# Performance work log

Measured on AMD Instinct MI355X. Metric: run time of the kernel, lower is better.

## Reference

```python
import jax, jax.numpy as jnp
import numpy as np

H = 16        # attention heads
KVH = 4       # kv heads (GQA)
D = 128       # qk head_dim = qk_nope(64) + qk_rope(64)
ROPE = 64     # rotary sub-dim
VCH = 128     # v_channels
HID = 2048    # hidden size
E = 8         # routed experts
K = 2         # top-k
EPS = 1e-6
THETA = 10000.0


def rmsnorm(x, w):
    return x * jax.lax.rsqrt(jnp.mean(x * x, axis=-1, keepdims=True) + EPS) * w


def apply_rope(x, pos):
    # x: [T, h, ROPE]; rotate-half convention on the rope sub-dim
    half = ROPE // 2
    inv_freq = 1.0 / (THETA ** (jnp.arange(half, dtype=jnp.float32) / half))
    ang = pos.astype(jnp.float32)[:, None] * inv_freq          # [T, half]
    cos = jnp.cos(ang)[:, None, :]
    sin = jnp.sin(ang)[:, None, :]
    x1, x2 = x[..., :half], x[..., half:]
    return jnp.concatenate([x1 * cos - x2 * sin, x1 * sin + x2 * cos], axis=-1)


def swiglu(x, w_gate, w_up, w_down):
    return (jax.nn.silu(x @ w_gate) * (x @ w_up)) @ w_down


def setup_inputs() -> dict:
    key = jax.random.key(0)
    ks = jax.random.split(key, 16)
    T = 2048
    sc = 0.02
    n = lambda k, s: jax.random.normal(k, s, dtype=jnp.float32) * sc
    return {
        "x": jax.random.normal(ks[0], (T, HID), dtype=jnp.float32),
        "positions": jnp.arange(T, dtype=jnp.int32),
        "ln1_w": jnp.ones((HID,), jnp.float32),
        "qkv_w": n(ks[1], (HID, H * D + KVH * D + KVH * VCH)),
        "qkv_b": n(ks[2], (H * D + KVH * D + KVH * VCH,)),
        "k_ln_w": jnp.ones((D,), jnp.float32),
        "o_w": n(ks[3], (H * VCH, HID)),
        "ln2_w": jnp.ones((HID,), jnp.float32),
        "router_w": n(ks[4], (HID, E)),
        "w1": n(ks[5], (E, HID, 512)),
        "w2": n(ks[6], (E, 512, HID)),
        "w3": n(ks[7], (E, HID, 512)),
        "sw1": n(ks[8], (HID, 1024)),
        "sw2": n(ks[9], (1024, HID)),
        "sw3": n(ks[10], (HID, 1024)),
    }


def reference(x, positions, ln1_w, qkv_w, qkv_b, k_ln_w, o_w, ln2_w,
              router_w, w1, w2, w3, sw1, sw2, sw3):
    T = x.shape[0]
    # --- attention block ---
    h = rmsnorm(x, ln1_w)
    qkv = h @ qkv_w + qkv_b
    q = qkv[:, : H * D].reshape(T, H, D)
    k = qkv[:, H * D : H * D + KVH * D].reshape(T, KVH, D)
    v = qkv[:, H * D + KVH * D :].reshape(T, KVH, VCH)
    k = rmsnorm(k, k_ln_w)  # per-head k_layernorm over head_dim
    # rope applied to the trailing qk_rope_dim of q/k
    q = jnp.concatenate([q[..., : D - ROPE], apply_rope(q[..., D - ROPE :], positions)], -1)
    k = jnp.concatenate([k[..., : D - ROPE], apply_rope(k[..., D - ROPE :], positions)], -1)
    rep = H // KVH
    kf = jnp.repeat(k, rep, axis=1)   # [T, H, D]
    vf = jnp.repeat(v, rep, axis=1)   # [T, H, VCH]
    scale = D ** -0.5
    scores = jnp.einsum("qhd,khd->hqk", q, kf) * scale
    causal = jnp.tril(jnp.ones((T, T), dtype=bool))
    scores = jnp.where(causal[None], scores, jnp.float32(-1e30))
    p = jax.nn.softmax(scores, axis=-1)
    attn = jnp.einsum("hqk,khv->qhv", p, vf).reshape(T, H * VCH)
    x = x + attn @ o_w
    # --- MoE block: shared expert + top-k routed experts ---
    h2 = rmsnorm(x, ln2_w)
    probs = jax.nn.softmax(h2 @ router_w, axis=-1)            # [T, E]
    topw, topi = jax.lax.top_k(probs, K)
    topw = topw / jnp.sum(topw, axis=-1, keepdims=True)        # renormalize top-k
    combine = jnp.sum(jax.nn.one_hot(topi, E, dtype=h2.dtype) * topw[..., None], axis=1)  # [T, E]
    moe = swiglu(h2, sw1, sw3, sw2)                            # shared expert
    for e in range(E):  # small fixed expert count
        moe = moe + combine[:, e : e + 1] * swiglu(h2, w1[e], w3[e], w2[e])
    return x + moe
```

## Files before the change

### kernel.cpp

```cpp
#include <hip/hip_runtime.h>


typedef _Float16 half_t;
typedef _Float16 half8 __attribute__((ext_vector_type(8)));
typedef float    f32x4 __attribute__((ext_vector_type(4)));
typedef float    floatx4 __attribute__((ext_vector_type(4)));

#define T_TOK 2048
#define HIDN  2048
#define NH    16
#define NKVH  4
#define HD    128
#define QKV_N 3072
#define NEXP  8

#define MFMA16(a,b,c) __builtin_amdgcn_mfma_f32_16x16x32_f16(a,b,c,0,0,0)

__device__ __forceinline__ void gload_lds16(const half_t* g, half_t* l) {
    __builtin_amdgcn_global_load_lds(
        (const __attribute__((address_space(1))) void*)g,
        (__attribute__((address_space(3))) void*)l, 16, 0, 0);
}

__global__ __launch_bounds__(256)
void rmsnorm_split_k(const float* __restrict__ x, const float* __restrict__ w,
                     half_t* __restrict__ hi, half_t* __restrict__ lo)
{
    const int row = blockIdx.x, tid = threadIdx.x;
    const float* xr = x + (size_t)row * HIDN;
    floatx4 v0 = *(const floatx4*)(xr + tid * 8);
    floatx4 v1 = *(const floatx4*)(xr + tid * 8 + 4);
    float ss = v0[0]*v0[0] + v0[1]*v0[1] + v0[2]*v0[2] + v0[3]*v0[3]
             + v1[0]*v1[0] + v1[1]*v1[1] + v1[2]*v1[2] + v1[3]*v1[3];
    for (int o = 32; o; o >>= 1) ss += __shfl_down(ss, o);
    __shared__ float red[4];
    if ((tid & 63) == 0) red[tid >> 6] = ss;
    __syncthreads();
    ss = red[0] + red[1] + red[2] + red[3];
    float rs = rsqrtf(ss * (1.0f / HIDN) + 1e-6f);
    floatx4 w0 = *(const floatx4*)(w + tid * 8);
    floatx4 w1 = *(const floatx4*)(w + tid * 8 + 4);
    float vv[8] = { v0[0]*w0[0], v0[1]*w0[1], v0[2]*w0[2], v0[3]*w0[3],
                    v1[0]*w1[0], v1[1]*w1[1], v1[2]*w1[2], v1[3]*w1[3] };
    half8 hv, lv;
#pragma unroll
    for (int j = 0; j < 8; ++j) {
        float o = vv[j] * rs;
        half_t h = (half_t)o;
        hv[j] = h;
        lv[j] = (half_t)((o - (float)h) * 1024.0f);
    }
    *(half8*)(hi + (size_t)row * HIDN + tid * 8) = hv;
    if (lo) *(half8*)(lo + (size_t)row * HIDN + tid * 8) = lv;
}

__global__ __launch_bounds__(256)
void transpose_split2(const float* __restrict__ src, half_t* __restrict__ dh,
                      half_t* __restrict__ dl, int sstride, int dstride)
{
    __shared__ float tile[32][36];
    const int n0 = blockIdx.x * 32, k0 = blockIdx.y * 32;
    const int tid = threadIdx.x;
    {
        int r = tid >> 3, c = (tid & 7) * 4;
        *(floatx4*)&tile[r][c] =
            *(const floatx4*)(src + (size_t)(k0 + r) * sstride + n0 + c);
    }
    __syncthreads();
    int n = tid & 31, g = tid >> 5, gg = g & 3;
    half8 hv;
    if (g < 4) {
#pragma unroll
        for (int j = 0; j < 8; ++j) hv[j] = (half_t)tile[gg * 8 + j][n];
        *(half8*)(dh + (size_t)(n0 + n) * dstride + k0 + gg * 8) = hv;
    } else {
#pragma unroll
        for (int j = 0; j < 8; ++j) {
            float v = tile[gg * 8 + j][n];
            half_t h = (half_t)v;
            hv[j] = (half_t)((v - (float)h) * 1024.0f);
        }
        *(half8*)(dl + (size_t)(n0 + n) * dstride + k0 + gg * 8) = hv;
    }
}

__global__ __launch_bounds__(256)
void transpose_f16(const float* __restrict__ src, half_t* __restrict__ dh,
                   int sstride, int dstride)
{
    __shared__ float tile[32][68];
    const int n0 = blockIdx.x * 64, k0 = blockIdx.y * 32;
    const int tid = threadIdx.x;
    {
        int r = tid >> 3, c = (tid & 7) * 4;
        const float* s = src + (size_t)(k0 + r) * sstride + n0;
        *(floatx4*)&tile[r][c]      = *(const floatx4*)(s + c);
        *(floatx4*)&tile[r][c + 32] = *(const floatx4*)(s + c + 32);
    }
    __syncthreads();
    int n = tid & 63, g = tid >> 6;
    half8 hv;
#pragma unroll
    for (int j = 0; j < 8; ++j) hv[j] = (half_t)tile[g * 8 + j][n];
    *(half8*)(dh + (size_t)(n0 + n) * dstride + k0 + g * 8) = hv;
}

__global__ __launch_bounds__(256)
void w13_transpose(const float* __restrict__ sw1, const float* __restrict__ w1,
                   const float* __restrict__ sw3, const float* __restrict__ w3,
                   half_t* __restrict__ dst)
{
    __shared__ float tile[32][68];
    const int n0 = blockIdx.x * 64, k0 = blockIdx.y * 32;
    const int tid = threadIdx.x;
    const float* base;
    int stride;
    if (n0 < 1024)      { base = sw1 + n0; stride = 1024; }
    else if (n0 < 5120) { int e = (n0 - 1024) >> 9;
                          base = w1 + (size_t)e * HIDN * 512 + ((n0 - 1024) & 511);
                          stride = 512; }
    else if (n0 < 6144) { base = sw3 + (n0 - 5120); stride = 1024; }
    else                { int e = (n0 - 6144) >> 9;
                          base = w3 + (size_t)e * HIDN * 512 + ((n0 - 6144) & 511);
                          stride = 512; }
    {
        int r = tid >> 3, c = (tid & 7) * 4;
        const float* s = base + (size_t)(k0 + r) * stride;
        *(floatx4*)&tile[r][c]      = *(const floatx4*)(s + c);
        *(floatx4*)&tile[r][c + 32] = *(const floatx4*)(s + c + 32);
    }
    __syncthreads();
    int n = tid & 63, g = tid >> 6;
    half8 hv;
#pragma unroll
    for (int j = 0; j < 8; ++j) hv[j] = (half_t)tile[g * 8 + j][n];
    *(half8*)(dst + (size_t)(n0 + n) * HIDN + k0 + g * 8) = hv;
}

__global__ __launch_bounds__(256)
void w2_transpose(const float* __restrict__ sw2, const float* __restrict__ w2,
                  half_t* __restrict__ dst)
{
    __shared__ float tile[32][68];
    const int n0 = blockIdx.x * 64, k0 = blockIdx.y * 32;
    const int tid = threadIdx.x;
    {
        int r = tid >> 3, c = (tid & 7) * 4;
        int k = k0 + r;
        const float* s;
        if (k < 1024) s = sw2 + (size_t)k * HIDN + n0;
        else {
            int e = (k - 1024) >> 9, kk = (k - 1024) & 511;
            s = w2 + ((size_t)e * 512 + kk) * HIDN + n0;
        }
        *(floatx4*)&tile[r][c]      = *(const floatx4*)(s + c);
        *(floatx4*)&tile[r][c + 32] = *(const floatx4*)(s + c + 32);
    }
    __syncthreads();
    int n = tid & 63, g = tid >> 6;
    half8 hv;
#pragma unroll
    for (int j = 0; j < 8; ++j) hv[j] = (half_t)tile[g * 8 + j][n];
    *(half8*)(dst + (size_t)(n0 + n) * 5120 + k0 + g * 8) = hv;
}

__global__ __launch_bounds__(256)
void owu_kernel(const float* __restrict__ ow, const float* __restrict__ ln2w,
                const float* __restrict__ rw, float* __restrict__ owu)
{
    const int k = blockIdx.x * 4 + (threadIdx.x >> 6);
    const int lane = threadIdx.x & 63;
    float acc[NEXP] = {};
    const float* row = ow + (size_t)k * HIDN;
#pragma unroll
    for (int j = 0; j < 8; ++j) {
        int c = j * 256 + lane * 4;
        floatx4 ov = *(const floatx4*)(row + c);
        floatx4 lw = *(const floatx4*)(ln2w + c);
#pragma unroll
        for (int i = 0; i < 4; ++i) {
            float s = ov[i] * lw[i];
            const float* rwc = rw + (size_t)(c + i) * NEXP;
#pragma unroll
            for (int e = 0; e < NEXP; ++e) acc[e] += s * rwc[e];
        }
    }
#pragma unroll
    for (int e = 0; e < NEXP; ++e)
        for (int o = 32; o; o >>= 1) acc[e] += __shfl_down(acc[e], o);
    if (lane == 0) {
#pragma unroll
        for (int e = 0; e < NEXP; ++e) owu[(size_t)k * NEXP + e] = acc[e];
    }
}

template<bool SPLIT, int BM>
__global__ __launch_bounds__(256, 2)
void gemm_f16(const half_t* __restrict__ Ah, const half_t* __restrict__ Al,
              const half_t* __restrict__ Bth, const half_t* __restrict__ Btl,
              const float* __restrict__ bias, const float* __restrict__ res,
              float* __restrict__ Cf, half_t* __restrict__ Ch,
              int M, int N, int K)
{
    constexpr int NBUF = SPLIT ? 2 : 1;
    constexpr int MR = BM / 32;
    __shared__ half_t As[NBUF][BM * 32];
    __shared__ half_t Bs[NBUF][128 * 32];
    const int tid = threadIdx.x, lane = tid & 63, wid = tid >> 6;
    const int l15 = lane & 15, l4 = lane >> 4;
    const int row0 = blockIdx.y * BM, col0 = blockIdx.x * 128;
    const int wr = (wid >> 1) * (BM / 2), wc = (wid & 1) * 64;
    f32x4 accM[MR][4] = {}, accC[MR][4] = {};
    const int lrw = lane >> 2, lcl = (lane & 3) * 8;

    for (int k0 = 0; k0 < K; k0 += 32) {
        __syncthreads();
#pragma unroll
        for (int j = 0; j < BM / 64; ++j) {
            const int r = wid * (BM / 4) + j * 16;
            const size_t ga = (size_t)(row0 + r + lrw) * K + k0 + lcl;
            gload_lds16(Ah + ga, &As[0][r * 32]);
            if constexpr (SPLIT) gload_lds16(Al + ga, &As[1][r * 32]);
        }
#pragma unroll
        for (int j = 0; j < 2; ++j) {
            const int r = wid * 32 + j * 16;
            const size_t gb = (size_t)(col0 + r + lrw) * K + k0 + lcl;
            gload_lds16(Bth + gb, &Bs[0][r * 32]);
            if constexpr (SPLIT) gload_lds16(Btl + gb, &Bs[1][r * 32]);
        }
        __syncthreads();
        half8 ah[MR], al[MR], bh[4], bl[4];
#pragma unroll
        for (int m = 0; m < MR; ++m) {
            int off = (wr + m * 16 + l15) * 32 + l4 * 8;
            ah[m] = *(const half8*)&As[0][off];
            if constexpr (SPLIT) al[m] = *(const half8*)&As[1][off];
        }
#pragma unroll
        for (int n = 0; n < 4; ++n) {
            int off = (wc + n * 16 + l15) * 32 + l4 * 8;
            bh[n] = *(const half8*)&Bs[0][off];
            if constexpr (SPLIT) bl[n] = *(const half8*)&Bs[1][off];
        }
#pragma unroll
        for (int m = 0; m < MR; ++m)
#pragma unroll
            for (int n = 0; n < 4; ++n) {
                accM[m][n] = MFMA16(ah[m], bh[n], accM[m][n]);
                if constexpr (SPLIT) {
                    accC[m][n] = MFMA16(ah[m], bl[n], accC[m][n]);
                    accC[m][n] = MFMA16(al[m], bh[n], accC[m][n]);
                }
            }
    }
#pragma unroll
    for (int m = 0; m < MR; ++m) {
#pragma unroll
        for (int n = 0; n < 4; ++n) {
            int gr0 = row0 + wr + m * 16 + l4 * 4;
            int gc  = col0 + wc + n * 16 + l15;
            float b = bias ? bias[gc] : 0.0f;
#pragma unroll
            for (int i = 0; i < 4; ++i) {
                float v = accM[m][n][i];
                if constexpr (SPLIT) v += accC[m][n][i] * (1.0f / 1024.0f);
                v += b;
                size_t idx = (size_t)(gr0 + i) * N + gc;
                if (res) v += res[idx];
                if (Cf) Cf[idx] = v;
                if (Ch) Ch[idx] = (half_t)v;
            }
        }
    }
}

__global__ __launch_bounds__(256)
void qkv_prep(const float* __restrict__ qkv, const int* __restrict__ pos,
              const float* __restrict__ klnw,
              half_t* __restrict__ qh, half_t* __restrict__ ql,
              half_t* __restrict__ kh, half_t* __restrict__ kl)
{
    const int t = blockIdx.x, tid = threadIdx.x, lane = tid & 63, wid = tid >> 6;
    const float* row = qkv + (size_t)t * QKV_N;
    __shared__ float cs[32], sn[32];
    if (tid < 32) {
        double freq = exp((double)tid * -0.28782313662425572);
        double ang = (double)pos[t] * freq;
        const double twopi = 6.283185307179586476925286766559;
        ang -= twopi * floor(ang * (1.0 / twopi));
        float a = (float)ang;
        cs[tid] = cosf(a);
        sn[tid] = sinf(a);
    }
    __syncthreads();

    const float qscale = 0.08838834764831845f;
    {
        const int hh = tid >> 4, d0 = (tid & 15) * 8;
        const float* qrow = row + hh * HD;
        float outv[8];
        if (d0 < 64) {
#pragma unroll
            for (int j = 0; j < 8; ++j) outv[j] = qrow[d0 + j];
        } else if (d0 < 96) {
            int j0 = d0 - 64;
#pragma unroll
            for (int j = 0; j < 8; ++j) {
                int jj = j0 + j;
                outv[j] = qrow[64 + jj] * cs[jj] - qrow[96 + jj] * sn[jj];
            }
        } else {
            int j0 = d0 - 96;
#pragma unroll
            for (int j = 0; j < 8; ++j) {
                int jj = j0 + j;
                outv[j] = qrow[64 + jj] * sn[jj] + qrow[96 + jj] * cs[jj];
            }
        }
        half8 hv, lv;
#pragma unroll
        for (int j = 0; j < 8; ++j) {
            float o = outv[j] * qscale;
            half_t h = (half_t)o;
            hv[j] = h;
            lv[j] = (half_t)((o - (float)h) * 1024.0f);
        }
        size_t base = (size_t)t * (NH * HD) + hh * HD + d0;
        *(half8*)(qh + base) = hv;
        *(half8*)(ql + base) = lv;
    }
    {
        const float* krow = row + NH * HD + wid * HD;
        float a0 = krow[lane], a1 = krow[64 + lane];
        float ss = a0 * a0 + a1 * a1;
        for (int o = 32; o; o >>= 1) ss += __shfl_down(ss, o);
        ss = __shfl(ss, 0);
        float rs = rsqrtf(ss * (1.0f / HD) + 1e-6f);
        float n0 = a0 * rs * klnw[lane];
        float n1 = a1 * rs * klnw[64 + lane];
        float other = __shfl_xor(n1, 32);
        int j = lane & 31;
        float o1 = (lane < 32) ? (n1 * cs[j] - other * sn[j])
                               : (other * sn[j] + n1 * cs[j]);
        size_t base = (size_t)t * (NKVH * HD) + wid * HD;
        half_t h;
        h = (half_t)n0; kh[base + lane] = h;
        kl[base + lane] = (half_t)((n0 - (float)h) * 1024.0f);
        h = (half_t)o1; kh[base + 64 + lane] = h;
        kl[base + 64 + lane] = (half_t)((o1 - (float)h) * 1024.0f);
    }
}

__global__ __launch_bounds__(256, 2)
void attn_kernel(const half_t* __restrict__ qh, const half_t* __restrict__ ql,
                 const half_t* __restrict__ kh, const half_t* __restrict__ kl,
                 const half_t* __restrict__ vth, const half_t* __restrict__ vtl,
                 half_t* __restrict__ oh, half_t* __restrict__ ol)
{
    const int bid = blockIdx.x;
    const int qblk = 31 - (bid >> 4);
    const int h = bid & 15;
    const int kvh = h >> 2;
    const int tid = threadIdx.x, lane = tid & 63, wid = tid >> 6;
    const int q0 = qblk * 64 + wid * 16;
    const int l15 = lane & 15, l4 = lane >> 4;

    __shared__ half_t Ksh[32][136], Ksl[32][136];
    __shared__ half_t Vsh[128][40], Vsl[128][40];
    __shared__ half_t Ph[4][16][40], Pl[4][16][40];

    half8 qfh[4], qfl[4];
    {
        const size_t qb = (size_t)(q0 + l15) * (NH * HD) + h * HD + l4 * 8;
#pragma unroll
        for (int c = 0; c < 4; ++c) {
            qfh[c] = *(const half8*)(qh + qb + c * 32);
            qfl[c] = *(const half8*)(ql + qb + c * 32);
        }
    }

    f32x4 om[8] = {}, oc[8] = {};
    float mrow[4] = { -1e30f, -1e30f, -1e30f, -1e30f };
    float lrow[4] = {};

    const int kr = tid >> 4, kc = (tid & 15) * 8;
    const int vd = tid >> 2, vc = (tid & 3) * 8;
    uint4 rk0h, rk1h, rk0l, rk1l, rv0h, rv1h, rv0l, rv1l;

    const int kvend = qblk * 64 + 64;

#define LOAD_TILE(KV0)                                                        \
    do {                                                                      \
        size_t sk0 = (size_t)((KV0) + kr) * (NKVH * HD) + kvh * HD + kc;      \
        size_t sk1 = sk0 + (size_t)16 * (NKVH * HD);                          \
        rk0h = *(const uint4*)(kh + sk0);  rk0l = *(const uint4*)(kl + sk0);  \
        rk1h = *(const uint4*)(kh + sk1);  rk1l = *(const uint4*)(kl + sk1);  \
        size_t sv0 = (size_t)(kvh * HD + vd) * T_TOK + (KV0) + vc;            \
        size_t sv1 = sv0 + (size_t)64 * T_TOK;                                \
        rv0h = *(const uint4*)(vth + sv0); rv0l = *(const uint4*)(vtl + sv0); \
        rv1h = *(const uint4*)(vth + sv1); rv1l = *(const uint4*)(vtl + sv1); \
    } while (0)

    LOAD_TILE(0);
    for (int kv0 = 0; kv0 < kvend; kv0 += 32) {
        *(uint4*)&Ksh[kr][kc]      = rk0h;  *(uint4*)&Ksl[kr][kc]      = rk0l;
        *(uint4*)&Ksh[kr + 16][kc] = rk1h;  *(uint4*)&Ksl[kr + 16][kc] = rk1l;
        *(uint4*)&Vsh[vd][vc]      = rv0h;  *(uint4*)&Vsl[vd][vc]      = rv0l;
        *(uint4*)&Vsh[vd + 64][vc] = rv1h;  *(uint4*)&Vsl[vd + 64][vc] = rv1l;
        __syncthreads();
        if (kv0 + 32 < kvend) LOAD_TILE(kv0 + 32);

        f32x4 sf[2];
        __builtin_amdgcn_s_setprio(1);
#pragma unroll
        for (int t2 = 0; t2 < 2; ++t2) {
            f32x4 s = {}, sc = {};
#pragma unroll
            for (int c = 0; c < 4; ++c) {
                half8 bh = *(const half8*)&Ksh[t2 * 16 + l15][c * 32 + l4 * 8];
                half8 bl = *(const half8*)&Ksl[t2 * 16 + l15][c * 32 + l4 * 8];
                s  = MFMA16(qfh[c], bh, s);
                sc = MFMA16(qfh[c], bl, sc);
                sc = MFMA16(qfl[c], bh, sc);
            }
            sf[t2] = s + sc * (1.0f / 1024.0f);
        }
        __builtin_amdgcn_s_setprio(0);

        float pmax[4];
#pragma unroll
        for (int i = 0; i < 4; ++i) {
            const int qg = q0 + l4 * 4 + i;
#pragma unroll
            for (int t2 = 0; t2 < 2; ++t2) {
                int kvg = kv0 + t2 * 16 + l15;
                if (kvg > qg) sf[t2][i] = -1e30f;
            }
            float mx = fmaxf(sf[0][i], sf[1][i]);
#pragma unroll
            for (int o = 1; o < 16; o <<= 1) mx = fmaxf(mx, __shfl_xor(mx, o));
            pmax[i] = mx;
        }
        float dm = fmaxf(fmaxf(pmax[0] - mrow[0], pmax[1] - mrow[1]),
                         fmaxf(pmax[2] - mrow[2], pmax[3] - mrow[3]));
        if (__any(dm > 6.0f)) {
#pragma unroll
            for (int i = 0; i < 4; ++i) {
                float mnew = fmaxf(mrow[i], pmax[i]);
                float resc = expf(mrow[i] - mnew);
                lrow[i] *= resc;
#pragma unroll
                for (int c8 = 0; c8 < 8; ++c8) {
                    om[c8][i] *= resc; oc[c8][i] *= resc;
                }
                mrow[i] = mnew;
            }
        }
#pragma unroll
        for (int i = 0; i < 4; ++i) {
            float p0 = expf(sf[0][i] - mrow[i]);
            float p1 = expf(sf[1][i] - mrow[i]);
            lrow[i] += p0 + p1;
            half_t hh;
            hh = (half_t)p0;
            Ph[wid][l4 * 4 + i][l15] = hh;
            Pl[wid][l4 * 4 + i][l15] = (half_t)((p0 - (float)hh) * 1024.0f);
            hh = (half_t)p1;
            Ph[wid][l4 * 4 + i][16 + l15] = hh;
            Pl[wid][l4 * 4 + i][16 + l15] = (half_t)((p1 - (float)hh) * 1024.0f);
        }

        half8 pah = *(const half8*)&Ph[wid][l15][l4 * 8];
        half8 pal = *(const half8*)&Pl[wid][l15][l4 * 8];
        __builtin_amdgcn_s_setprio(1);
#pragma unroll
        for (int c8 = 0; c8 < 8; ++c8) {
            half8 vh = *(const half8*)&Vsh[c8 * 16 + l15][l4 * 8];
            half8 vl = *(const half8*)&Vsl[c8 * 16 + l15][l4 * 8];
            om[c8] = MFMA16(pah, vh, om[c8]);
            oc[c8] = MFMA16(pah, vl, oc[c8]);
            oc[c8] = MFMA16(pal, vh, oc[c8]);
        }
        __builtin_amdgcn_s_setprio(0);
        __syncthreads();
    }
#undef LOAD_TILE

#pragma unroll
    for (int i = 0; i < 4; ++i)
#pragma unroll
        for (int o = 1; o < 16; o <<= 1) lrow[i] += __shfl_xor(lrow[i], o);

#pragma unroll
    for (int c8 = 0; c8 < 8; ++c8) {
#pragma unroll
        for (int i = 0; i < 4; ++i) {
            float v = (om[c8][i] + oc[c8][i] * (1.0f / 1024.0f)) / lrow[i];
            size_t idx = (size_t)(q0 + l4 * 4 + i) * (NH * HD) + h * HD + c8 * 16 + l15;
            half_t hh = (half_t)v;
            oh[idx] = hh;
            ol[idx] = (half_t)((v - (float)hh) * 1024.0f);
        }
    }
}

__global__ __launch_bounds__(256)
void router_linear(const float* __restrict__ x, const half_t* __restrict__ ah,
                   const half_t* __restrict__ al, const float* __restrict__ x2,
                   const float* __restrict__ ln2w, const float* __restrict__ rw,
                   const float* __restrict__ owu, float* __restrict__ combine)
{
    const int t = blockIdx.x, tid = threadIdx.x;
    const float* xr2 = x2 + (size_t)t * HIDN;
    float ss = 0.0f;
#pragma unroll
    for (int i = 0; i < 8; ++i) {
        float v = xr2[tid + i * 256];
        ss += v * v;
    }
    for (int o = 32; o; o >>= 1) ss += __shfl_down(ss, o);
    __shared__ float red[4];
    if ((tid & 63) == 0) red[tid >> 6] = ss;
    __syncthreads();
    ss = red[0] + red[1] + red[2] + red[3];
    float rs = rsqrtf(ss * (1.0f / HIDN) + 1e-6f);

    const float* xr = x + (size_t)t * HIDN;
    const half_t* ar = ah + (size_t)t * HIDN;
    const half_t* alr = al + (size_t)t * HIDN;
    float acc[NEXP] = {};
#pragma unroll
    for (int i = 0; i < 8; ++i) {
        int c = tid + i * 256;
        float xv = xr[c] * ln2w[c];
        float ap = (float)ar[c] + (float)alr[c] * (1.0f / 1024.0f);
        const float* rwc = rw + (size_t)c * NEXP;
        const float* owc = owu + (size_t)c * NEXP;
#pragma unroll
        for (int e = 0; e < NEXP; ++e) acc[e] += xv * rwc[e] + ap * owc[e];
    }
#pragma unroll
    for (int e = 0; e < NEXP; ++e)
        for (int o = 32; o; o >>= 1) acc[e] += __shfl_down(acc[e], o);
    __shared__ float red8[4][NEXP];
    if ((tid & 63) == 0)
#pragma unroll
        for (int e = 0; e < NEXP; ++e) red8[tid >> 6][e] = acc[e];
    __syncthreads();
    if (tid == 0) {
        float lg[NEXP];
#pragma unroll
        for (int e = 0; e < NEXP; ++e)
            lg[e] = (red8[0][e] + red8[1][e] + red8[2][e] + red8[3][e]) * rs;
        int i1 = 0;
        for (int e = 1; e < NEXP; ++e) if (lg[e] > lg[i1]) i1 = e;
        int i2 = (i1 == 0) ? 1 : 0;
        for (int e = 0; e < NEXP; ++e) if (e != i1 && lg[e] > lg[i2]) i2 = e;
        float mx = lg[i1];
        float p1 = expf(lg[i1] - mx), p2 = expf(lg[i2] - mx);
        float inv = 1.0f / (p1 + p2);
        float* cr = combine + (size_t)t * NEXP;
#pragma unroll
        for (int e = 0; e < NEXP; ++e) cr[e] = 0.0f;
        cr[i1] = p1 * inv;
        cr[i2] = p2 * inv;
    }
}

__global__ __launch_bounds__(256)
void moe_act(const half_t* __restrict__ GU, const float* __restrict__ comb,
             half_t* __restrict__ Abig)
{
    int idx = blockIdx.x * 256 + threadIdx.x;
    int t = idx / 640, c8 = idx % 640;
    int n = c8 * 8;
    half8 g8 = *(const half8*)(GU + (size_t)t * 10240 + n);
    half8 u8 = *(const half8*)(GU + (size_t)t * 10240 + 5120 + n);
    float sc = (n < 1024) ? 1.0f : comb[(size_t)t * NEXP + ((n - 1024) >> 9)];
    half8 o8;
#pragma unroll
    for (int j = 0; j < 8; ++j) {
        float g = (float)g8[j], u = (float)u8[j];
        float s = g / (1.0f + expf(-g));
        o8[j] = (half_t)(s * u * sc);
    }
    *(half8*)(Abig + (size_t)t * 5120 + n) = o8;
}

extern "C" void kernel_launch(void* const* d_in, const int* in_sizes, int n_in,
                              void* d_out, int out_size, void* d_ws, size_t ws_size,
                              hipStream_t stream)
{
    (void)in_sizes; (void)n_in; (void)out_size; (void)ws_size;
    const float* x    = (const float*)d_in[0];
    const int*   pos  = (const int*)  d_in[1];
    const float* ln1w = (const float*)d_in[2];
    const float* qkvw = (const float*)d_in[3];
    const float* qkvb = (const float*)d_in[4];
    const float* klnw = (const float*)d_in[5];
    const float* ow   = (const float*)d_in[6];
    const float* ln2w = (const float*)d_in[7];
    const float* rw   = (const float*)d_in[8];
    const float* w1   = (const float*)d_in[9];
    const float* w2   = (const float*)d_in[10];
    const float* w3   = (const float*)d_in[11];
    const float* sw1  = (const float*)d_in[12];
    const float* sw2  = (const float*)d_in[13];
    const float* sw3  = (const float*)d_in[14];
    float* out = (float*)d_out;

    char* ws = (char*)d_ws;
    const size_t AB = 16842752;
    float*  x2      = (float*)(ws);
    float*  combine = (float*)(ws + 16777216);
    half_t* h_hi    = (half_t*)(ws + AB);
    half_t* h_lo    = (half_t*)(ws + AB + 8388608);
    half_t* qkvwt_h = (half_t*)(ws + AB + 16777216);
    half_t* qkvwt_l = (half_t*)(ws + AB + 29360128);
    float*  qkv     = (float*)(ws + AB + 41943040);
    half_t* q_h     = (half_t*)(ws + AB + 67108864);
    half_t* q_l     = (half_t*)(ws + AB + 75497472);
    half_t* k_h     = (half_t*)(ws + AB + 83886080);
    half_t* k_l     = (half_t*)(ws + AB + 85983232);
    half_t* vt_h    = (half_t*)(ws + AB + 88080384);
    half_t* vt_l    = (half_t*)(ws + AB + 90177536);
    half_t* attn_h  = (half_t*)(ws + AB);
    half_t* attn_l  = (half_t*)(ws + AB + 8388608);
    half_t* owt     = (half_t*)(ws + AB + 16777216);
    float*  ow_u    = (float*)(ws + AB + 25165824);
    half_t* h2      = (half_t*)(ws + AB + 33554432);
    half_t* W13t    = (half_t*)(ws + AB + 41943040);
    half_t* GU      = (half_t*)(ws + AB + 83886080);
    half_t* Abig    = (half_t*)(ws + AB);
    half_t* W2t     = (half_t*)(ws + AB + 41943040);

    dim3 b256(256);

    rmsnorm_split_k<<<T_TOK, b256, 0, stream>>>(x, ln1w, h_hi, h_lo);
    transpose_split2<<<dim3(QKV_N / 32, HIDN / 32), b256, 0, stream>>>(
        qkvw, qkvwt_h, qkvwt_l, QKV_N, HIDN);
    gemm_f16<true, 64><<<dim3(QKV_N / 128, T_TOK / 64), b256, 0, stream>>>(
        h_hi, h_lo, qkvwt_h, qkvwt_l, qkvb, nullptr, qkv, nullptr,
        T_TOK, QKV_N, HIDN);
    qkv_prep<<<T_TOK, b256, 0, stream>>>(qkv, pos, klnw, q_h, q_l, k_h, k_l);
    transpose_split2<<<dim3(512 / 32, T_TOK / 32), b256, 0, stream>>>(
        qkv + 2560, vt_h, vt_l, QKV_N, T_TOK);
    transpose_f16<<<dim3(HIDN / 64, HIDN / 32), b256, 0, stream>>>(
        ow, owt, HIDN, HIDN);
    owu_kernel<<<512, b256, 0, stream>>>(ow, ln2w, rw, ow_u);
    attn_kernel<<<512, b256, 0, stream>>>(
        q_h, q_l, k_h, k_l, vt_h, vt_l, attn_h, attn_l);
    gemm_f16<false, 64><<<dim3(HIDN / 128, T_TOK / 64), b256, 0, stream>>>(
        attn_h, nullptr, owt, nullptr, nullptr, x, x2, nullptr,
        T_TOK, HIDN, HIDN);
    router_linear<<<T_TOK, b256, 0, stream>>>(
        x, attn_h, attn_l, x2, ln2w, rw, ow_u, combine);
    rmsnorm_split_k<<<T_TOK, b256, 0, stream>>>(x2, ln2w, h2, nullptr);
    w13_transpose<<<dim3(10240 / 64, HIDN / 32), b256, 0, stream>>>(
        sw1, w1, sw3, w3, W13t);
    gemm_f16<false, 128><<<dim3(10240 / 128, T_TOK / 128), b256, 0, stream>>>(
        h2, nullptr, W13t, nullptr, nullptr, nullptr, nullptr, GU,
        T_TOK, 10240, HIDN);
    w2_transpose<<<dim3(HIDN / 64, 5120 / 32), b256, 0, stream>>>(sw2, w2, W2t);
    moe_act<<<(T_TOK * 640) / 256, b256, 0, stream>>>(GU, combine, Abig);
    gemm_f16<false, 64><<<dim3(HIDN / 128, T_TOK / 64), b256, 0, stream>>>(
        Abig, nullptr, W2t, nullptr, nullptr, x2, out, nullptr,
        T_TOK, HIDN, 5120);
}
```

Baseline: 648.9 us.

## Double-buffer GEMM LDS loads and split causal attention over KV chunks

The GEMM kernel now double-buffers its LDS tiles so the next K-slice's global-to-LDS load is issued before the current slice's MFMAs, and it takes an occupancy template parameter. Attention is split-K over 512-wide KV chunks. Later query blocks are spread across up to 4 blocks, which balances causal work across 1280 blocks, and a new combine kernel merges the partials with log-sum-exp rescaling. The split adds fp32 partial traffic, an extra launch, and workspace aliasing that could conflict with other buffers. Launch bounds also change for attention and some GEMMs, which affects register pressure.

```diff
diff --git a/kernel.cpp b/kernel.cpp
--- a/kernel.cpp
+++ b/kernel.cpp
@@ -194,8 +194,8 @@
     }
 }
 
-template<bool SPLIT, int BM>
-__global__ __launch_bounds__(256, 2)
+template<bool SPLIT, int BM, int WPE>
+__global__ __launch_bounds__(256, WPE)
 void gemm_f16(const half_t* __restrict__ Ah, const half_t* __restrict__ Al,
               const half_t* __restrict__ Bth, const half_t* __restrict__ Btl,
               const float* __restrict__ bias, const float* __restrict__ res,
@@ -204,8 +204,8 @@
 {
     constexpr int NBUF = SPLIT ? 2 : 1;
     constexpr int MR = BM / 32;
-    __shared__ half_t As[NBUF][BM * 32];
-    __shared__ half_t Bs[NBUF][128 * 32];
+    __shared__ half_t As[2][NBUF][BM * 32];
+    __shared__ half_t Bs[2][NBUF][128 * 32];
     const int tid = threadIdx.x, lane = tid & 63, wid = tid >> 6;
     const int l15 = lane & 15, l4 = lane >> 4;
     const int row0 = blockIdx.y * BM, col0 = blockIdx.x * 128;
@@ -213,35 +213,41 @@
     f32x4 accM[MR][4] = {}, accC[MR][4] = {};
     const int lrw = lane >> 2, lcl = (lane & 3) * 8;
 
-    for (int k0 = 0; k0 < K; k0 += 32) {
-        __syncthreads();
-#pragma unroll
-        for (int j = 0; j < BM / 64; ++j) {
-            const int r = wid * (BM / 4) + j * 16;
-            const size_t ga = (size_t)(row0 + r + lrw) * K + k0 + lcl;
-            gload_lds16(Ah + ga, &As[0][r * 32]);
-            if constexpr (SPLIT) gload_lds16(Al + ga, &As[1][r * 32]);
-        }
-#pragma unroll
-        for (int j = 0; j < 2; ++j) {
-            const int r = wid * 32 + j * 16;
-            const size_t gb = (size_t)(col0 + r + lrw) * K + k0 + lcl;
-            gload_lds16(Bth + gb, &Bs[0][r * 32]);
-            if constexpr (SPLIT) gload_lds16(Btl + gb, &Bs[1][r * 32]);
-        }
-        __syncthreads();
+#define STAGE(BUF, K0)                                                        \
+    do {                                                                      \
+        _Pragma("unroll")                                                     \
+        for (int j = 0; j < BM / 64; ++j) {                                   \
+            const int r = wid * (BM / 4) + j * 16;                            \
+            const size_t ga = (size_t)(row0 + r + lrw) * K + (K0) + lcl;      \
+            gload_lds16(Ah + ga, &As[BUF][0][r * 32]);                        \
+            if constexpr (SPLIT) gload_lds16(Al + ga, &As[BUF][1][r * 32]);   \
+        }                                                                     \
+        _Pragma("unroll")                                                     \
+        for (int j = 0; j < 2; ++j) {                                         \
+            const int r = wid * 32 + j * 16;                                  \
+            const size_t gb = (size_t)(col0 + r + lrw) * K + (K0) + lcl;      \
+            gload_lds16(Bth + gb, &Bs[BUF][0][r * 32]);                       \
+            if constexpr (SPLIT) gload_lds16(Btl + gb, &Bs[BUF][1][r * 32]);  \
+        }                                                                     \
+    } while (0)
+
+    STAGE(0, 0);
+    __syncthreads();
+    int cur = 0;
+    for (int k0 = 0; k0 < K; k0 += 32, cur ^= 1) {
+        if (k0 + 32 < K) STAGE(cur ^ 1, k0 + 32);
         half8 ah[MR], al[MR], bh[4], bl[4];
 #pragma unroll
         for (int m = 0; m < MR; ++m) {
             int off = (wr + m * 16 + l15) * 32 + l4 * 8;
-            ah[m] = *(const half8*)&As[0][off];
-            if constexpr (SPLIT) al[m] = *(const half8*)&As[1][off];
+            ah[m] = *(const half8*)&As[cur][0][off];
+            if constexpr (SPLIT) al[m] = *(const half8*)&As[cur][1][off];
         }
 #pragma unroll
         for (int n = 0; n < 4; ++n) {
             int off = (wc + n * 16 + l15) * 32 + l4 * 8;
-            bh[n] = *(const half8*)&Bs[0][off];
-            if constexpr (SPLIT) bl[n] = *(const half8*)&Bs[1][off];
+            bh[n] = *(const half8*)&Bs[cur][0][off];
+            if constexpr (SPLIT) bl[n] = *(const half8*)&Bs[cur][1][off];
         }
 #pragma unroll
         for (int m = 0; m < MR; ++m)
@@ -253,7 +259,10 @@
                     accC[m][n] = MFMA16(al[m], bh[n], accC[m][n]);
                 }
             }
-    }
+        __syncthreads();
+    }
+#undef STAGE
+
 #pragma unroll
     for (int m = 0; m < MR; ++m) {
 #pragma unroll
@@ -352,18 +361,28 @@
     }
 }
 
-__global__ __launch_bounds__(256, 2)
+__global__ __launch_bounds__(256, 3)
 void attn_kernel(const half_t* __restrict__ qh, const half_t* __restrict__ ql,
                  const half_t* __restrict__ kh, const half_t* __restrict__ kl,
                  const half_t* __restrict__ vth, const half_t* __restrict__ vtl,
-                 half_t* __restrict__ oh, half_t* __restrict__ ol)
+                 half_t* __restrict__ oh, half_t* __restrict__ ol,
+                 float* __restrict__ Op0, float* __restrict__ Op1,
+                 float* __restrict__ ml)
 {
     const int bid = blockIdx.x;
-    const int qblk = 31 - (bid >> 4);
-    const int h = bid & 15;
+    const int h = bid & 15, r = bid >> 4;
+    int q, c;
+    if (r < 8)       { q = r;                 c = 0; }
+    else if (r < 24) { q = 8 + ((r - 8) >> 1);  c = (r - 8) & 1; }
+    else if (r < 48) { q = 16 + (r - 24) / 3;   c = (r - 24) % 3; }
+    else             { q = 24 + ((r - 48) >> 2); c = (r - 48) & 3; }
+    const int nch = (q < 8) ? 1 : (q < 16) ? 2 : (q < 24) ? 3 : 4;
+    const int kvbeg = c * 512;
+    const int kvend = min(kvbeg + 512, q * 64 + 64);
+
     const int kvh = h >> 2;
     const int tid = threadIdx.x, lane = tid & 63, wid = tid >> 6;
-    const int q0 = qblk * 64 + wid * 16;
+    const int q0 = q * 64 + wid * 16;
     const int l15 = lane & 15, l4 = lane >> 4;
 
     __shared__ half_t Ksh[32][136], Ksl[32][136];
@@ -374,9 +393,9 @@
     {
         const size_t qb = (size_t)(q0 + l15) * (NH * HD) + h * HD + l4 * 8;
 #pragma unroll
-        for (int c = 0; c < 4; ++c) {
-            qfh[c] = *(const half8*)(qh + qb + c * 32);
-            qfl[c] = *(const half8*)(ql + qb + c * 32);
+        for (int cc = 0; cc < 4; ++cc) {
+            qfh[cc] = *(const half8*)(qh + qb + cc * 32);
+            qfl[cc] = *(const half8*)(ql + qb + cc * 32);
         }
     }
 
@@ -387,8 +406,6 @@
     const int kr = tid >> 4, kc = (tid & 15) * 8;
     const int vd = tid >> 2, vc = (tid & 3) * 8;
     uint4 rk0h, rk1h, rk0l, rk1l, rv0h, rv1h, rv0l, rv1l;
-
-    const int kvend = qblk * 64 + 64;
 
 #define LOAD_TILE(KV0)                                                        \
     do {                                                                      \
@@ -402,8 +419,8 @@
         rv1h = *(const uint4*)(vth + sv1); rv1l = *(const uint4*)(vtl + sv1); \
     } while (0)
 
-    LOAD_TILE(0);
-    for (int kv0 = 0; kv0 < kvend; kv0 += 32) {
+    LOAD_TILE(kvbeg);
+    for (int kv0 = kvbeg; kv0 < kvend; kv0 += 32) {
         *(uint4*)&Ksh[kr][kc]      = rk0h;  *(uint4*)&Ksl[kr][kc]      = rk0l;
         *(uint4*)&Ksh[kr + 16][kc] = rk1h;  *(uint4*)&Ksl[kr + 16][kc] = rk1l;
         *(uint4*)&Vsh[vd][vc]      = rv0h;  *(uint4*)&Vsl[vd][vc]      = rv0l;
@@ -417,12 +434,12 @@
         for (int t2 = 0; t2 < 2; ++t2) {
             f32x4 s = {}, sc = {};
 #pragma unroll
-            for (int c = 0; c < 4; ++c) {
-                half8 bh = *(const half8*)&Ksh[t2 * 16 + l15][c * 32 + l4 * 8];
-                half8 bl = *(const half8*)&Ksl[t2 * 16 + l15][c * 32 + l4 * 8];
-                s  = MFMA16(qfh[c], bh, s);
-                sc = MFMA16(qfh[c], bl, sc);
-                sc = MFMA16(qfl[c], bh, sc);
+            for (int cc = 0; cc < 4; ++cc) {
+                half8 bh = *(const half8*)&Ksh[t2 * 16 + l15][cc * 32 + l4 * 8];
+                half8 bl = *(const half8*)&Ksl[t2 * 16 + l15][cc * 32 + l4 * 8];
+                s  = MFMA16(qfh[cc], bh, s);
+                sc = MFMA16(qfh[cc], bl, sc);
+                sc = MFMA16(qfl[cc], bh, sc);
             }
             sf[t2] = s + sc * (1.0f / 1024.0f);
         }
@@ -492,16 +509,98 @@
 #pragma unroll
         for (int o = 1; o < 16; o <<= 1) lrow[i] += __shfl_xor(lrow[i], o);
 
-#pragma unroll
-    for (int c8 = 0; c8 < 8; ++c8) {
-#pragma unroll
-        for (int i = 0; i < 4; ++i) {
-            float v = (om[c8][i] + oc[c8][i] * (1.0f / 1024.0f)) / lrow[i];
-            size_t idx = (size_t)(q0 + l4 * 4 + i) * (NH * HD) + h * HD + c8 * 16 + l15;
-            half_t hh = (half_t)v;
-            oh[idx] = hh;
-            ol[idx] = (half_t)((v - (float)hh) * 1024.0f);
-        }
+    if (nch == 1) {
+#pragma unroll
+        for (int c8 = 0; c8 < 8; ++c8) {
+#pragma unroll
+            for (int i = 0; i < 4; ++i) {
+                float v = (om[c8][i] + oc[c8][i] * (1.0f / 1024.0f)) / lrow[i];
+                size_t idx = (size_t)(q0 + l4 * 4 + i) * (NH * HD) + h * HD
+                           + c8 * 16 + l15;
+                half_t hh = (half_t)v;
+                oh[idx] = hh;
+                ol[idx] = (half_t)((v - (float)hh) * 1024.0f);
+            }
+        }
+    } else {
+        float* Op = (bid < 768) ? Op0 + (size_t)bid * 8192
+                                : Op1 + (size_t)(bid - 768) * 8192;
+#pragma unroll
+        for (int c8 = 0; c8 < 8; ++c8) {
+#pragma unroll
+            for (int i = 0; i < 4; ++i) {
+                int row64 = wid * 16 + l4 * 4 + i;
+                Op[row64 * 128 + c8 * 16 + l15] =
+                    om[c8][i] + oc[c8][i] * (1.0f / 1024.0f);
+            }
+        }
+        if (l15 == 0) {
+#pragma unroll
+            for (int i = 0; i < 4; ++i) {
+                int row64 = wid * 16 + l4 * 4 + i;
+                ml[(size_t)bid * 128 + row64]      = mrow[i];
+                ml[(size_t)bid * 128 + 64 + row64] = lrow[i];
+            }
+        }
+    }
+}
+
+__global__ __launch_bounds__(256)
+void attn_combine(const float* __restrict__ Op0, const float* __restrict__ Op1,
+                  const float* __restrict__ ml,
+                  half_t* __restrict__ oh, half_t* __restrict__ ol)
+{
+    const int bid = blockIdx.x;
+    const int h = bid & 15, q = 8 + (bid >> 4);
+    const int nch = (q < 16) ? 2 : (q < 24) ? 3 : 4;
+    const int r0 = (q < 16) ? 8 + (q - 8) * 2
+                 : (q < 24) ? 24 + (q - 16) * 3
+                            : 48 + (q - 24) * 4;
+    const int tid = threadIdx.x;
+    const int row = tid >> 2, cg = (tid & 3) * 32;
+
+    const float* Oc[4];
+    float m[4], lv[4];
+#pragma unroll
+    for (int c = 0; c < 4; ++c) {
+        int cc = (c < nch) ? c : nch - 1;
+        int slot = (r0 + cc) * 16 + h;
+        const float* base = (slot < 768) ? Op0 + (size_t)slot * 8192
+                                         : Op1 + (size_t)(slot - 768) * 8192;
+        Oc[c] = base + row * 128 + cg;
+        m[c]  = ml[(size_t)slot * 128 + row];
+        lv[c] = (c < nch) ? ml[(size_t)slot * 128 + 64 + row] : 0.0f;
+    }
+    float M = fmaxf(fmaxf(m[0], m[1]), fmaxf(m[2], m[3]));
+    float w[4], wsum = 0.0f;
+#pragma unroll
+    for (int c = 0; c < 4; ++c) { w[c] = expf(m[c] - M); wsum += lv[c] * w[c]; }
+    float inv = 1.0f / wsum;
+    float wO[4];
+#pragma unroll
+    for (int c = 0; c < 4; ++c) wO[c] = (c < nch) ? w[c] * inv : 0.0f;
+
+    size_t obase = (size_t)(q * 64 + row) * (NH * HD) + h * HD + cg;
+#pragma unroll
+    for (int jj = 0; jj < 4; ++jj) {
+        floatx4 a0 = {0,0,0,0}, a1 = {0,0,0,0};
+#pragma unroll
+        for (int c = 0; c < 4; ++c) {
+            floatx4 v0 = *(const floatx4*)(Oc[c] + jj * 8);
+            floatx4 v1 = *(const floatx4*)(Oc[c] + jj * 8 + 4);
+            a0 += wO[c] * v0;
+            a1 += wO[c] * v1;
+        }
+        half8 hv, lvv;
+#pragma unroll
+        for (int k = 0; k < 4; ++k) {
+            half_t hh = (half_t)a0[k];
+            hv[k] = hh; lvv[k] = (half_t)((a0[k] - (float)hh) * 1024.0f);
+            hh = (half_t)a1[k];
+            hv[4 + k] = hh; lvv[4 + k] = (half_t)((a1[k] - (float)hh) * 1024.0f);
+        }
+        *(half8*)(oh + obase + jj * 8) = hv;
+        *(half8*)(ol + obase + jj * 8) = lvv;
     }
 }
 
@@ -629,6 +728,9 @@
     half_t* attn_l  = (half_t*)(ws + AB + 8388608);
     half_t* owt     = (half_t*)(ws + AB + 16777216);
     float*  ow_u    = (float*)(ws + AB + 25165824);
+    float*  mlpart  = (float*)(ws + AB + 25231360);
+    float*  Opart0  = (float*)(ws + AB + 41943040);
+    float*  Opart1  = (float*)(ws);
     half_t* h2      = (half_t*)(ws + AB + 33554432);
     half_t* W13t    = (half_t*)(ws + AB + 41943040);
     half_t* GU      = (half_t*)(ws + AB + 83886080);
@@ -640,7 +742,7 @@
     rmsnorm_split_k<<<T_TOK, b256, 0, stream>>>(x, ln1w, h_hi, h_lo);
     transpose_split2<<<dim3(QKV_N / 32, HIDN / 32), b256, 0, stream>>>(
         qkvw, qkvwt_h, qkvwt_l, QKV_N, HIDN);
-    gemm_f16<true, 64><<<dim3(QKV_N / 128, T_TOK / 64), b256, 0, stream>>>(
+    gemm_f16<true, 64, 3><<<dim3(QKV_N / 128, T_TOK / 64), b256, 0, stream>>>(
         h_hi, h_lo, qkvwt_h, qkvwt_l, qkvb, nullptr, qkv, nullptr,
         T_TOK, QKV_N, HIDN);
     qkv_prep<<<T_TOK, b256, 0, stream>>>(qkv, pos, klnw, q_h, q_l, k_h, k_l);
@@ -649,9 +751,12 @@
     transpose_f16<<<dim3(HIDN / 64, HIDN / 32), b256, 0, stream>>>(
         ow, owt, HIDN, HIDN);
     owu_kernel<<<512, b256, 0, stream>>>(ow, ln2w, rw, ow_u);
-    attn_kernel<<<512, b256, 0, stream>>>(
-        q_h, q_l, k_h, k_l, vt_h, vt_l, attn_h, attn_l);
-    gemm_f16<false, 64><<<dim3(HIDN / 128, T_TOK / 64), b256, 0, stream>>>(
+    attn_kernel<<<1280, b256, 0, stream>>>(
+        q_h, q_l, k_h, k_l, vt_h, vt_l, attn_h, attn_l,
+        Opart0, Opart1, mlpart);
+    attn_combine<<<384, b256, 0, stream>>>(Opart0, Opart1, mlpart,
+                                           attn_h, attn_l);
+    gemm_f16<false, 64, 2><<<dim3(HIDN / 128, T_TOK / 64), b256, 0, stream>>>(
         attn_h, nullptr, owt, nullptr, nullptr, x, x2, nullptr,
         T_TOK, HIDN, HIDN);
     router_linear<<<T_TOK, b256, 0, stream>>>(
@@ -659,12 +764,12 @@
     rmsnorm_split_k<<<T_TOK, b256, 0, stream>>>(x2, ln2w, h2, nullptr);
     w13_transpose<<<dim3(10240 / 64, HIDN / 32), b256, 0, stream>>>(
         sw1, w1, sw3, w3, W13t);
-    gemm_f16<false, 128><<<dim3(10240 / 128, T_TOK / 128), b256, 0, stream>>>(
+    gemm_f16<false, 128, 3><<<dim3(10240 / 128, T_TOK / 128), b256, 0, stream>>>(
         h2, nullptr, W13t, nullptr, nullptr, nullptr, nullptr, GU,
         T_TOK, 10240, HIDN);
     w2_transpose<<<dim3(HIDN / 64, 5120 / 32), b256, 0, stream>>>(sw2, w2, W2t);
     moe_act<<<(T_TOK * 640) / 256, b256, 0, stream>>>(GU, combine, Abig);
-    gemm_f16<false, 64><<<dim3(HIDN / 128, T_TOK / 64), b256, 0, stream>>>(
+    gemm_f16<false, 64, 2><<<dim3(HIDN / 128, T_TOK / 64), b256, 0, stream>>>(
         Abig, nullptr, W2t, nullptr, nullptr, x2, out, nullptr,
         T_TOK, HIDN, 5120);
 }
```

Result: slower. 724.4 us (+11.6%).
